# Kernel tuning notes

Hardware: AMD Instinct MI355X
Metric: run time of the kernel (lower is better)

## Reference

```python
import jax, jax.numpy as jnp
import numpy as np

N = 16384          # merged batch*time tokens
K = 5              # num mixture components
D = 1088           # latent_dim (1024) + vec dim (64)


def setup_inputs() -> dict:
    key = jax.random.key(0)
    k1, k2, k3, k4 = jax.random.split(key, 4)
    return {
        "target": jax.random.normal(k1, (N, D), dtype=jnp.float32),
        "s_mean": jax.random.normal(k2, (N, K * D), dtype=jnp.float32),
        "s_logstd": jax.random.normal(k3, (N, K * D), dtype=jnp.float32),
        "log_mix_coeffs": jax.random.normal(k4, (N, K), dtype=jnp.float32),
    }


def reference(target, s_mean, s_logstd, log_mix_coeffs):
    # torch.chunk(x, K, dim=-1) then stack(dim=1) == reshape to [N, K, D]
    n, kd = s_mean.shape
    k = log_mix_coeffs.shape[-1]
    d = kd // k
    means = s_mean.reshape(n, k, d)      # [N, K, D]
    logstds = s_logstd.reshape(n, k, d)  # [N, K, D]
    # per-component unnormalized Gaussian log-density (as in original _step)
    z = (target[:, None, :] - means) / jnp.exp(logstds)   # [N, K, D]
    logp = -0.5 * jnp.sum(z * z, axis=-1) - jnp.sum(logstds, axis=-1)  # [N, K]
    loss = -jax.nn.logsumexp(log_mix_coeffs + logp, axis=1).mean()
    return loss
```

## Files before the change

kernel.cpp:

```cpp
#include <hip/hip_runtime.h>
#include <math.h>

namespace {

typedef float f32x4 __attribute__((ext_vector_type(4)));

constexpr int KC  = 5;
constexpr int DIM = 1088;
constexpr int D4  = DIM / 4;
constexpr int FULL_IT = D4 / 64;
constexpr int REM     = D4 % 64;

__global__ void zero_out_kernel(float* out) { out[0] = 0.0f; }

__global__ __launch_bounds__(512) void mdn_loss_kernel(
    const float* __restrict__ target,
    const float* __restrict__ s_mean,
    const float* __restrict__ s_logstd,
    const float* __restrict__ log_mix,
    float* __restrict__ out,
    int n_rows, float inv_n)
{
    const int wave_in_block = threadIdx.x >> 6;
    const int lane          = threadIdx.x & 63;
    const int row           = blockIdx.x * (blockDim.x >> 6) + wave_in_block;

    float row_loss = 0.0f;

    if (row < n_rows) {
        const f32x4* tg = reinterpret_cast<const f32x4*>(target) + (size_t)row * D4;

        f32x4 t[FULL_IT + 1];
        #pragma unroll
        for (int i = 0; i < FULL_IT; ++i)
            t[i] = __builtin_nontemporal_load(tg + lane + i * 64);
        if (lane < REM)
            t[FULL_IT] = __builtin_nontemporal_load(tg + lane + FULL_IT * 64);

        const f32x4* mrow = reinterpret_cast<const f32x4*>(s_mean)   + (size_t)row * (KC * D4);
        const f32x4* lrow = reinterpret_cast<const f32x4*>(s_logstd) + (size_t)row * (KC * D4);

        float a[KC];
        #pragma unroll 1
        for (int k = 0; k < KC; ++k) {
            const f32x4* mk = mrow + k * D4;
            const f32x4* lk = lrow + k * D4;

            f32x4 m[FULL_IT + 1], l[FULL_IT + 1];
            #pragma unroll
            for (int i = 0; i < FULL_IT; ++i) {
                m[i] = __builtin_nontemporal_load(mk + lane + i * 64);
                l[i] = __builtin_nontemporal_load(lk + lane + i * 64);
            }
            if (lane < REM) {
                m[FULL_IT] = __builtin_nontemporal_load(mk + lane + FULL_IT * 64);
                l[FULL_IT] = __builtin_nontemporal_load(lk + lane + FULL_IT * 64);
            }

            float z2a = 0.0f, z2b = 0.0f, lsa = 0.0f, lsb = 0.0f;
            #pragma unroll
            for (int i = 0; i < FULL_IT; ++i) {
                float r0 = (t[i].x - m[i].x) * __expf(-l[i].x);
                float r1 = (t[i].y - m[i].y) * __expf(-l[i].y);
                float r2 = (t[i].z - m[i].z) * __expf(-l[i].z);
                float r3 = (t[i].w - m[i].w) * __expf(-l[i].w);
                z2a = fmaf(r0, r0, z2a);  lsa += l[i].x;
                z2b = fmaf(r1, r1, z2b);  lsb += l[i].y;
                z2a = fmaf(r2, r2, z2a);  lsa += l[i].z;
                z2b = fmaf(r3, r3, z2b);  lsb += l[i].w;
            }
            if (lane < REM) {
                float r0 = (t[FULL_IT].x - m[FULL_IT].x) * __expf(-l[FULL_IT].x);
                float r1 = (t[FULL_IT].y - m[FULL_IT].y) * __expf(-l[FULL_IT].y);
                float r2 = (t[FULL_IT].z - m[FULL_IT].z) * __expf(-l[FULL_IT].z);
                float r3 = (t[FULL_IT].w - m[FULL_IT].w) * __expf(-l[FULL_IT].w);
                z2a = fmaf(r0, r0, z2a);  lsa += l[FULL_IT].x;
                z2b = fmaf(r1, r1, z2b);  lsb += l[FULL_IT].y;
                z2a = fmaf(r2, r2, z2a);  lsa += l[FULL_IT].z;
                z2b = fmaf(r3, r3, z2b);  lsb += l[FULL_IT].w;
            }
            float z2 = z2a + z2b, lsum = lsa + lsb;

            #pragma unroll
            for (int off = 32; off; off >>= 1) {
                z2   += __shfl_xor(z2, off);
                lsum += __shfl_xor(lsum, off);
            }
            a[k] = -0.5f * z2 - lsum;
        }

        if (lane == 0) {
            const float* lm = log_mix + (size_t)row * KC;
            float mx = -INFINITY;
            #pragma unroll
            for (int k = 0; k < KC; ++k) { a[k] += lm[k]; mx = fmaxf(mx, a[k]); }
            float s = 0.0f;
            #pragma unroll
            for (int k = 0; k < KC; ++k) s += __expf(a[k] - mx);
            row_loss = -(mx + __logf(s)) * inv_n;
        }
    }

    __shared__ float part[8];
    if (lane == 0) part[wave_in_block] = row_loss;
    __syncthreads();
    if (threadIdx.x == 0) {
        float s = 0.0f;
        #pragma unroll
        for (int w = 0; w < 8; ++w) s += part[w];
        atomicAdd(out, s);
    }
}

}

extern "C" void kernel_launch(void* const* d_in, const int* in_sizes, int n_in,
                              void* d_out, int out_size, void* d_ws, size_t ws_size,
                              hipStream_t stream)
{
    const float* target   = (const float*)d_in[0];
    const float* s_mean   = (const float*)d_in[1];
    const float* s_logstd = (const float*)d_in[2];
    const float* log_mix  = (const float*)d_in[3];
    float* out = (float*)d_out;

    const int n_rows = in_sizes[0] / DIM;

    zero_out_kernel<<<1, 1, 0, stream>>>(out);

    const int waves_per_block = 8;
    const int blocks = (n_rows + waves_per_block - 1) / waves_per_block;
    mdn_loss_kernel<<<blocks, 512, 0, stream>>>(target, s_mean, s_logstd, log_mix,
                                                out, n_rows, 1.0f / n_rows);
}
```

Measured before the change: 132.4 us.

## Replace global atomic accumulation with per-block partials and a reduction kernel

Each block now writes its partial loss sum to workspace, and a small second kernel reduces those partials, replacing the zero-init kernel plus 2048 atomicAdds on one address. The per-row log-mix coefficients are loaded early by all lanes. The two wave reductions are merged into one shuffle chain by folding 0.5*z2+lsum before the reduction. The load order is also regrouped into means then logstds. This removes atomic contention and halves the shuffle work, at the cost of depending on workspace availability and an extra tiny launch.

```diff
diff --git a/kernel.cpp b/kernel.cpp
--- a/kernel.cpp
+++ b/kernel.cpp
@@ -10,6 +10,7 @@
 constexpr int D4  = DIM / 4;
 constexpr int FULL_IT = D4 / 64;
 constexpr int REM     = D4 % 64;
+constexpr int WPB     = 8;
 
 __global__ void zero_out_kernel(float* out) { out[0] = 0.0f; }
 
@@ -19,15 +20,21 @@
     const float* __restrict__ s_logstd,
     const float* __restrict__ log_mix,
     float* __restrict__ out,
-    int n_rows, float inv_n)
+    float* __restrict__ partials,
+    int n_rows, float inv_n, int use_partials)
 {
     const int wave_in_block = threadIdx.x >> 6;
     const int lane          = threadIdx.x & 63;
-    const int row           = blockIdx.x * (blockDim.x >> 6) + wave_in_block;
+    const int row           = blockIdx.x * WPB + wave_in_block;
 
     float row_loss = 0.0f;
 
     if (row < n_rows) {
+        const float* lmp = log_mix + (size_t)row * KC;
+        float lm[KC];
+        #pragma unroll
+        for (int k = 0; k < KC; ++k) lm[k] = lmp[k];
+
         const f32x4* tg = reinterpret_cast<const f32x4*>(target) + (size_t)row * D4;
 
         f32x4 t[FULL_IT + 1];
@@ -48,14 +55,15 @@
 
             f32x4 m[FULL_IT + 1], l[FULL_IT + 1];
             #pragma unroll
-            for (int i = 0; i < FULL_IT; ++i) {
+            for (int i = 0; i < FULL_IT; ++i)
                 m[i] = __builtin_nontemporal_load(mk + lane + i * 64);
+            if (lane < REM)
+                m[FULL_IT] = __builtin_nontemporal_load(mk + lane + FULL_IT * 64);
+            #pragma unroll
+            for (int i = 0; i < FULL_IT; ++i)
                 l[i] = __builtin_nontemporal_load(lk + lane + i * 64);
-            }
-            if (lane < REM) {
-                m[FULL_IT] = __builtin_nontemporal_load(mk + lane + FULL_IT * 64);
+            if (lane < REM)
                 l[FULL_IT] = __builtin_nontemporal_load(lk + lane + FULL_IT * 64);
-            }
 
             float z2a = 0.0f, z2b = 0.0f, lsa = 0.0f, lsb = 0.0f;
             #pragma unroll
@@ -79,37 +87,44 @@
                 z2a = fmaf(r2, r2, z2a);  lsa += l[FULL_IT].z;
                 z2b = fmaf(r3, r3, z2b);  lsb += l[FULL_IT].w;
             }
-            float z2 = z2a + z2b, lsum = lsa + lsb;
-
+            float c = fmaf(0.5f, z2a + z2b, lsa + lsb);
             #pragma unroll
-            for (int off = 32; off; off >>= 1) {
-                z2   += __shfl_xor(z2, off);
-                lsum += __shfl_xor(lsum, off);
-            }
-            a[k] = -0.5f * z2 - lsum;
+            for (int off = 32; off; off >>= 1) c += __shfl_xor(c, off);
+            a[k] = lm[k] - c;
         }
 
-        if (lane == 0) {
-            const float* lm = log_mix + (size_t)row * KC;
-            float mx = -INFINITY;
-            #pragma unroll
-            for (int k = 0; k < KC; ++k) { a[k] += lm[k]; mx = fmaxf(mx, a[k]); }
-            float s = 0.0f;
-            #pragma unroll
-            for (int k = 0; k < KC; ++k) s += __expf(a[k] - mx);
-            row_loss = -(mx + __logf(s)) * inv_n;
-        }
+        float mx = a[0];
+        #pragma unroll
+        for (int k = 1; k < KC; ++k) mx = fmaxf(mx, a[k]);
+        float s = 0.0f;
+        #pragma unroll
+        for (int k = 0; k < KC; ++k) s += __expf(a[k] - mx);
+        row_loss = -(mx + __logf(s)) * inv_n;
     }
 
-    __shared__ float part[8];
+    __shared__ float part[WPB];
     if (lane == 0) part[wave_in_block] = row_loss;
     __syncthreads();
     if (threadIdx.x == 0) {
         float s = 0.0f;
         #pragma unroll
-        for (int w = 0; w < 8; ++w) s += part[w];
-        atomicAdd(out, s);
+        for (int w = 0; w < WPB; ++w) s += part[w];
+        if (use_partials) partials[blockIdx.x] = s;
+        else              atomicAdd(out, s);
     }
+}
+
+__global__ __launch_bounds__(256) void reduce_partials_kernel(
+    const float* __restrict__ partials, float* __restrict__ out, int n)
+{
+    float s = 0.0f;
+    for (int i = threadIdx.x; i < n; i += 256) s += partials[i];
+    #pragma unroll
+    for (int off = 32; off; off >>= 1) s += __shfl_xor(s, off);
+    __shared__ float part[4];
+    if ((threadIdx.x & 63) == 0) part[threadIdx.x >> 6] = s;
+    __syncthreads();
+    if (threadIdx.x == 0) out[0] = part[0] + part[1] + part[2] + part[3];
 }
 
 }
@@ -125,11 +140,20 @@
     float* out = (float*)d_out;
 
     const int n_rows = in_sizes[0] / DIM;
+    const int blocks = (n_rows + WPB - 1) / WPB;
 
-    zero_out_kernel<<<1, 1, 0, stream>>>(out);
+    const bool use_partials = (d_ws != nullptr) &&
+                              (ws_size >= (size_t)blocks * sizeof(float));
 
-    const int waves_per_block = 8;
-    const int blocks = (n_rows + waves_per_block - 1) / waves_per_block;
-    mdn_loss_kernel<<<blocks, 512, 0, stream>>>(target, s_mean, s_logstd, log_mix,
-                                                out, n_rows, 1.0f / n_rows);
+    if (use_partials) {
+        mdn_loss_kernel<<<blocks, 512, 0, stream>>>(
+            target, s_mean, s_logstd, log_mix, out, (float*)d_ws,
+            n_rows, 1.0f / n_rows, 1);
+        reduce_partials_kernel<<<1, 256, 0, stream>>>((const float*)d_ws, out, blocks);
+    } else {
+        zero_out_kernel<<<1, 1, 0, stream>>>(out);
+        mdn_loss_kernel<<<blocks, 512, 0, stream>>>(
+            target, s_mean, s_logstd, log_mix, out, nullptr,
+            n_rows, 1.0f / n_rows, 0);
+    }
 }
```

New measurement: 123.2 us. 1.07x faster.
